# Performance work log

Measured on AMD Instinct MI355X. Metric: run time of the kernel, lower is better.

Reference implementation:

```python
import jax, jax.numpy as jnp
import numpy as np

D = 256
H = 4
HD = D // H


def setup_inputs() -> dict:
    key = jax.random.key(0)
    ks = jax.random.split(key, 12)
    A, T = 64, 512
    s = 1.0 / np.sqrt(D)
    return {
        "features": jax.random.normal(ks[0], (A, T, D), jnp.float32),
        "positions": jax.random.normal(ks[1], (A, T, 2), jnp.float32),
        "Wq": jax.random.normal(ks[2], (D, D), jnp.float32) * s,
        "bq": jnp.zeros((D,), jnp.float32),
        "Wk": jax.random.normal(ks[3], (D, D), jnp.float32) * s,
        "bk": jnp.zeros((D,), jnp.float32),
        "Wv": jax.random.normal(ks[4], (D, D), jnp.float32) * s,
        "bv": jnp.zeros((D,), jnp.float32),
        "Wo": jax.random.normal(ks[5], (D, D), jnp.float32) * s,
        "bo": jnp.zeros((D,), jnp.float32),
        "max_distance": 2,
        "time_window": 64,
    }


def _sparse_mask(positions, max_distance, time_window):
    # positions: [A, T, 2] -> allowed [A, T, T]
    A, T, _ = positions.shape
    diff = positions[:, :, None, :] - positions[:, None, :, :]  # [A,T,T,2]
    dist2 = jnp.sum(diff * diff, axis=-1)                       # [A,T,T]
    t = jnp.arange(T)
    tmask = jnp.abs(t[:, None] - t[None, :]) <= time_window      # [T,T]
    return (dist2 <= float(max_distance) ** 2) & tmask[None]     # [A,T,T]


def reference(features, positions, Wq, bq, Wk, bk, Wv, bv, Wo, bo,
              max_distance, time_window):
    A, T, Dm = features.shape
    allowed = _sparse_mask(positions, max_distance, time_window)  # [A,T,T]
    q = features @ Wq.T + bq
    k = features @ Wk.T + bk
    v = features @ Wv.T + bv
    # split heads: [A, T, H, HD]
    q = q.reshape(A, T, H, HD)
    k = k.reshape(A, T, H, HD)
    v = v.reshape(A, T, H, HD)
    scale = 1.0 / np.sqrt(HD)
    scores = jnp.einsum("athd,ashd->ahts", q, k) * scale          # [A,H,T,T]
    scores = jnp.where(allowed[:, None], scores, -jnp.inf)
    attn = jax.nn.softmax(scores, axis=-1)
    out = jnp.einsum("ahts,ashd->athd", attn, v).reshape(A, T, Dm)
    return out @ Wo.T + bo
```

## Files before the change

kernel.cpp:

```cpp
#include <hip/hip_runtime.h>
#include <hip/hip_bf16.h>
#include <cstdint>
#include <cstddef>

typedef __attribute__((ext_vector_type(8))) _Float16 half8;
typedef __attribute__((ext_vector_type(4))) float floatx4;

#define MFMA16(a, b, c) __builtin_amdgcn_mfma_f32_16x16x32_f16((a), (b), (c), 0, 0, 0)

#define GLOAD_LDS16(g, l)                                                     \
    __builtin_amdgcn_global_load_lds(                                         \
        (const __attribute__((address_space(1))) void*)(g),                   \
        (__attribute__((address_space(3))) void*)(l), 16, 0, 0)

#define NFEAT 8388608

__device__ __forceinline__ void stage_dma(
    const _Float16* __restrict__ src, _Float16* __restrict__ lds,
    int wid, int lane)
{
#pragma unroll
    for (int i = 0; i < 4; ++i) {
        int grp = wid * 4 + i;
        int row = grp * 8 + (lane >> 3);
        int sc  = (lane & 7) ^ (row & 7);
        GLOAD_LDS16(src + (size_t)row * 256 + sc * 8, lds + grp * 512);
    }
}

__device__ __forceinline__ void stage_f32_s(
    const float* __restrict__ src, _Float16* __restrict__ lds, int tid,
    int dst_stride)
{
#pragma unroll
    for (int i = 0; i < 4; ++i) {
        int g   = tid + 256 * i;
        int row = g >> 3, chd = g & 7;
        int chs = chd ^ (row & 7);
        const float* s = src + (size_t)row * 256 + chs * 8;
        float4 v0 = *(const float4*)s;
        float4 v1 = *(const float4*)(s + 4);
        half8 h = { (_Float16)v0.x, (_Float16)v0.y, (_Float16)v0.z, (_Float16)v0.w,
                    (_Float16)v1.x, (_Float16)v1.y, (_Float16)v1.z, (_Float16)v1.w };
        *(half8*)(&lds[row * dst_stride + chd * 8]) = h;
    }
}

__global__ __launch_bounds__(256) void qkv_fused(
    const float* __restrict__ feat,
    const float* __restrict__ Wq, const float* __restrict__ Wk,
    const float* __restrict__ Wv,
    const float* __restrict__ bq, const float* __restrict__ bk,
    const float* __restrict__ bv,
    _Float16* __restrict__ Qb, _Float16* __restrict__ Kb, _Float16* __restrict__ Vb)
{
    __shared__ _Float16 Xs[128 * 256];
    __shared__ _Float16 Ws[128 * 64];

    const int n   = blockIdx.x;
    const int idx = n >> 3;
    const int bm  = (n & 7) * 32 + (idx >> 1);
    const int bn  = idx & 1;

    const int tid  = threadIdx.x;
    const int lane = tid & 63, wid = tid >> 6;
    const int quad = lane >> 4, l16 = lane & 15;
    const int wm = wid & 1, wn = wid >> 1;

    const float* Xg = feat + (size_t)bm * 128 * 256;
#pragma unroll
    for (int slab = 0; slab < 4; ++slab)
        stage_f32_s(Xg + slab * 64, Xs + slab * 64, tid, 256);
    __syncthreads();

#pragma unroll 1
    for (int z = 0; z < 3; ++z) {
        const float* W    = (z == 0) ? Wq : (z == 1) ? Wk : Wv;
        const float* bias = (z == 0) ? bq : (z == 1) ? bk : bv;
        _Float16*    outp = (z == 0) ? Qb : (z == 1) ? Kb : Vb;
        const float* Wg = W + (size_t)bn * 128 * 256;

        floatx4 acc[4][4] = {};
#pragma unroll 1
        for (int ks = 0; ks < 4; ++ks) {
            stage_f32_s(Wg + ks * 64, Ws, tid, 64);
            __syncthreads();
#pragma unroll
            for (int kh = 0; kh < 2; ++kh) {
                half8 af[4], bf[4];
#pragma unroll
                for (int mi = 0; mi < 4; ++mi) {
                    int row = wm * 64 + mi * 16 + l16;
                    int cs  = (kh * 4 + quad) ^ (row & 7);
                    af[mi] = *(const half8*)(&Xs[row * 256 + ks * 64 + cs * 8]);
                }
#pragma unroll
                for (int ni = 0; ni < 4; ++ni) {
                    int row = wn * 64 + ni * 16 + l16;
                    int cs  = (kh * 4 + quad) ^ (row & 7);
                    bf[ni] = *(const half8*)(&Ws[row * 64 + cs * 8]);
                }
#pragma unroll
                for (int mi = 0; mi < 4; ++mi)
#pragma unroll
                    for (int ni = 0; ni < 4; ++ni)
                        acc[mi][ni] = MFMA16(af[mi], bf[ni], acc[mi][ni]);
            }
            __syncthreads();
        }

#pragma unroll
        for (int ni = 0; ni < 4; ++ni) {
            int col = bn * 128 + wn * 64 + ni * 16 + l16;
            float bv2 = bias[col];
#pragma unroll
            for (int mi = 0; mi < 4; ++mi)
#pragma unroll
                for (int r = 0; r < 4; ++r) {
                    int row = bm * 128 + wm * 64 + mi * 16 + quad * 4 + r;
                    outp[(size_t)row * 256 + col] = (_Float16)(acc[mi][ni][r] + bv2);
                }
        }
    }
}

__global__ __launch_bounds__(256) void out_gemm(
    const _Float16* __restrict__ attnH, const float* __restrict__ Wo,
    const float* __restrict__ bo, float* __restrict__ out)
{
    __shared__ _Float16 As[128 * 64];
    __shared__ _Float16 Bs[128 * 64];

    const int n   = blockIdx.x;
    const int idx = n >> 3;
    const int bm  = (n & 7) * 32 + (idx >> 1);
    const int bn  = idx & 1;

    const int tid  = threadIdx.x;
    const int lane = tid & 63, wid = tid >> 6;
    const int quad = lane >> 4, l16 = lane & 15;
    const int wm = wid & 1, wn = wid >> 1;

    floatx4 acc[4][4] = {};
    const float* Wg = Wo + (size_t)bn * 128 * 256;

    for (int k0 = 0; k0 < 256; k0 += 64) {
        stage_dma(attnH + (size_t)bm * 128 * 256 + k0, As, wid, lane);
        stage_f32_s(Wg + k0, Bs, tid, 64);
        __syncthreads();
#pragma unroll
        for (int kh = 0; kh < 2; ++kh) {
            half8 af[4], bf[4];
#pragma unroll
            for (int mi = 0; mi < 4; ++mi) {
                int row = wm * 64 + mi * 16 + l16;
                int cs  = (kh * 4 + quad) ^ (row & 7);
                af[mi] = *(const half8*)(&As[row * 64 + cs * 8]);
            }
#pragma unroll
            for (int ni = 0; ni < 4; ++ni) {
                int row = wn * 64 + ni * 16 + l16;
                int cs  = (kh * 4 + quad) ^ (row & 7);
                bf[ni] = *(const half8*)(&Bs[row * 64 + cs * 8]);
            }
#pragma unroll
            for (int mi = 0; mi < 4; ++mi)
#pragma unroll
                for (int ni = 0; ni < 4; ++ni)
                    acc[mi][ni] = MFMA16(af[mi], bf[ni], acc[mi][ni]);
        }
        __syncthreads();
    }

#pragma unroll
    for (int ni = 0; ni < 4; ++ni) {
        int col = bn * 128 + wn * 64 + ni * 16 + l16;
        float bv = bo[col];
#pragma unroll
        for (int mi = 0; mi < 4; ++mi)
#pragma unroll
            for (int r = 0; r < 4; ++r) {
                int row = bm * 128 + wm * 64 + mi * 16 + quad * 4 + r;
                out[(size_t)row * 256 + col] = acc[mi][ni][r] + bv;
            }
    }
}

__global__ __launch_bounds__(256) void attn_kernel(
    const _Float16* __restrict__ Qb, const _Float16* __restrict__ Kb,
    const _Float16* __restrict__ Vb, const float* __restrict__ positions,
    const int* __restrict__ mdp, const int* __restrict__ twp,
    _Float16* __restrict__ attnb)
{
    const int n   = blockIdx.x;
    const int idx = n >> 3;
    const int a   = (n & 7) * 8 + (idx >> 5);
    const int rem = idx & 31;
    const int qt  = rem >> 2, h = rem & 3;

    const int q0 = qt * 64;
    const int s_base = q0 - 64;
    const int tid = threadIdx.x, lane = tid & 63, wid = tid >> 6;
    const int quad = lane >> 4, l16 = lane & 15;

    __shared__ _Float16 KPs[192 * 64];
    __shared__ _Float16 Vt[64 * 192];

    const size_t abase = (size_t)a * 512;
    const int md = *mdp, tw = *twp;
    const float md2 = (float)(md * md);

    const size_t qrow = abase + q0 + wid * 16 + l16;
    half8 aq0 = *(const half8*)(Qb + qrow * 256 + h * 64 + quad * 8);
    half8 aq1 = *(const half8*)(Qb + qrow * 256 + h * 64 + 32 + quad * 8);
    float qpx[4], qpy[4];
    int trow[4];
#pragma unroll
    for (int r = 0; r < 4; ++r) {
        int m = wid * 16 + quad * 4 + r;
        trow[r] = q0 + m;
        float2 qp = *(const float2*)(positions + (abase + q0 + m) * 2);
        qpx[r] = qp.x;
        qpy[r] = qp.y;
    }

#pragma unroll
    for (int i = 0; i < 6; ++i) {
        int grp = wid * 6 + i;
        int si  = grp * 8 + (lane >> 3);
        int sc  = min(max(s_base + si, 0), 511);
        int ch  = (lane & 7) ^ (si & 7);
        GLOAD_LDS16(Kb + (abase + sc) * 256 + h * 64 + ch * 8, KPs + grp * 512);
    }
#pragma unroll
    for (int i = 0; i < 3; ++i) {
        int g   = tid + 256 * i;
        int si2 = (g % 96) * 2;
        int d0  = (g / 96) * 8;
        int sa  = min(max(s_base + si2, 0), 511);
        int sb  = min(max(s_base + si2 + 1, 0), 511);
        half8 v0 = *(const half8*)(Vb + (abase + sa) * 256 + h * 64 + d0);
        half8 v1 = *(const half8*)(Vb + (abase + sb) * 256 + h * 64 + d0);
        int c = si2 >> 3;
#pragma unroll
        for (int j = 0; j < 8; ++j) {
            int d  = d0 + j;
            int cs = (c & ~7) | ((c & 7) ^ (d & 7));
            union { _Float16 hh[2]; uint32_t u; } p;
            p.hh[0] = v0[j]; p.hh[1] = v1[j];
            *(uint32_t*)(&Vt[d * 192 + cs * 8 + (si2 & 7)]) = p.u;
        }
    }
    __syncthreads();

    floatx4 S[12];
#pragma unroll
    for (int j = 0; j < 12; ++j) {
        int si = j * 16 + l16;
        half8 bk0 = *(const half8*)(&KPs[si * 64 + ((quad) ^ (si & 7)) * 8]);
        half8 bk1 = *(const half8*)(&KPs[si * 64 + ((4 + quad) ^ (si & 7)) * 8]);
        floatx4 acc = {};
        acc = MFMA16(aq0, bk0, acc);
        acc = MFMA16(aq1, bk1, acc);
        int sr = s_base + si;
        int sc = min(max(sr, 0), 511);
        float2 kp = *(const float2*)(positions + (abase + sc) * 2);
        bool svalid = (sr >= 0) && (sr < 512);
#pragma unroll
        for (int r = 0; r < 4; ++r) {
            float dx = qpx[r] - kp.x, dy = qpy[r] - kp.y;
            float d2 = dx * dx + dy * dy;
            int dt = trow[r] - sr; dt = dt < 0 ? -dt : dt;
            bool ok = svalid && (d2 <= md2) && (dt <= tw);
            S[j][r] = ok ? acc[r] * 0.125f : -1e30f;
        }
    }

    float minv[4];
#pragma unroll
    for (int r = 0; r < 4; ++r) {
        float m = -1e30f;
#pragma unroll
        for (int j = 0; j < 12; ++j) m = fmaxf(m, S[j][r]);
        m = fmaxf(m, __shfl_xor(m, 1));
        m = fmaxf(m, __shfl_xor(m, 2));
        m = fmaxf(m, __shfl_xor(m, 4));
        m = fmaxf(m, __shfl_xor(m, 8));
        float l = 0.f;
#pragma unroll
        for (int j = 0; j < 12; ++j) {
            float p = __expf(S[j][r] - m);
            S[j][r] = p;
            l += p;
        }
        l += __shfl_xor(l, 1);
        l += __shfl_xor(l, 2);
        l += __shfl_xor(l, 4);
        l += __shfl_xor(l, 8);
        minv[r] = 1.0f / l;
    }

    __syncthreads();

    _Float16* Ps = KPs + wid * (16 * 192);
#pragma unroll
    for (int j = 0; j < 12; ++j)
#pragma unroll
        for (int r = 0; r < 4; ++r) {
            int row = quad * 4 + r;
            int col = j * 16 + l16;
            int ch  = (col >> 3) ^ (row & 7);
            Ps[row * 192 + ch * 8 + (col & 7)] = (_Float16)(S[j][r] * minv[r]);
        }

    half8 af[6];
#pragma unroll
    for (int k = 0; k < 6; ++k) {
        int ch = (k * 4 + quad) ^ (l16 & 7);
        af[k] = *(const half8*)(&Ps[l16 * 192 + ch * 8]);
    }
#pragma unroll
    for (int nn = 0; nn < 4; ++nn) {
        floatx4 accO = {};
#pragma unroll
        for (int k = 0; k < 6; ++k) {
            int row = nn * 16 + l16;
            int c   = k * 4 + quad;
            int cs  = (c & ~7) | ((c & 7) ^ (row & 7));
            half8 bv = *(const half8*)(&Vt[row * 192 + cs * 8]);
            accO = MFMA16(af[k], bv, accO);
        }
#pragma unroll
        for (int r = 0; r < 4; ++r) {
            int row = q0 + wid * 16 + quad * 4 + r;
            attnb[(abase + row) * 256 + h * 64 + nn * 16 + l16] = (_Float16)accO[r];
        }
    }
}

extern "C" void kernel_launch(void* const* d_in, const int* in_sizes, int n_in,
                              void* d_out, int out_size, void* d_ws, size_t ws_size,
                              hipStream_t stream)
{
    const float* feat = (const float*)d_in[0];
    const float* pos  = (const float*)d_in[1];
    const float* Wq   = (const float*)d_in[2];
    const float* bq   = (const float*)d_in[3];
    const float* Wk   = (const float*)d_in[4];
    const float* bk   = (const float*)d_in[5];
    const float* Wv   = (const float*)d_in[6];
    const float* bv   = (const float*)d_in[7];
    const float* Wo   = (const float*)d_in[8];
    const float* bo   = (const float*)d_in[9];
    const int*   md   = (const int*)d_in[10];
    const int*   tw   = (const int*)d_in[11];
    float*       out  = (float*)d_out;

    _Float16* ws    = (_Float16*)d_ws;
    _Float16* Qb    = ws;
    _Float16* Kb    = Qb + NFEAT;
    _Float16* Vb    = Kb + NFEAT;
    _Float16* attnH = Vb + NFEAT;

    qkv_fused<<<512, 256, 0, stream>>>(feat, Wq, Wk, Wv, bq, bk, bv, Qb, Kb, Vb);

    attn_kernel<<<2048, 256, 0, stream>>>(Qb, Kb, Vb, pos, md, tw, attnH);

    out_gemm<<<512, 256, 0, stream>>>(attnH, Wo, bo, out);
}
```

Baseline: 167.7 us.

## Software-pipeline weight tile loads through registers in QKV and output GEMMs

```diff
diff --git a/kernel.cpp b/kernel.cpp
--- a/kernel.cpp
+++ b/kernel.cpp
@@ -14,37 +14,6 @@
         (__attribute__((address_space(3))) void*)(l), 16, 0, 0)
 
 #define NFEAT 8388608
-
-__device__ __forceinline__ void stage_dma(
-    const _Float16* __restrict__ src, _Float16* __restrict__ lds,
-    int wid, int lane)
-{
-#pragma unroll
-    for (int i = 0; i < 4; ++i) {
-        int grp = wid * 4 + i;
-        int row = grp * 8 + (lane >> 3);
-        int sc  = (lane & 7) ^ (row & 7);
-        GLOAD_LDS16(src + (size_t)row * 256 + sc * 8, lds + grp * 512);
-    }
-}
-
-__device__ __forceinline__ void stage_f32_s(
-    const float* __restrict__ src, _Float16* __restrict__ lds, int tid,
-    int dst_stride)
-{
-#pragma unroll
-    for (int i = 0; i < 4; ++i) {
-        int g   = tid + 256 * i;
-        int row = g >> 3, chd = g & 7;
-        int chs = chd ^ (row & 7);
-        const float* s = src + (size_t)row * 256 + chs * 8;
-        float4 v0 = *(const float4*)s;
-        float4 v1 = *(const float4*)(s + 4);
-        half8 h = { (_Float16)v0.x, (_Float16)v0.y, (_Float16)v0.z, (_Float16)v0.w,
-                    (_Float16)v1.x, (_Float16)v1.y, (_Float16)v1.z, (_Float16)v1.w };
-        *(half8*)(&lds[row * dst_stride + chd * 8]) = h;
-    }
-}
 
 __global__ __launch_bounds__(256) void qkv_fused(
     const float* __restrict__ feat,
@@ -54,7 +23,7 @@
     const float* __restrict__ bv,
     _Float16* __restrict__ Qb, _Float16* __restrict__ Kb, _Float16* __restrict__ Vb)
 {
-    __shared__ _Float16 Xs[128 * 256];
+    __shared__ _Float16 Xs[4 * 128 * 64];
     __shared__ _Float16 Ws[128 * 64];
 
     const int n   = blockIdx.x;
@@ -69,57 +38,105 @@
 
     const float* Xg = feat + (size_t)bm * 128 * 256;
 #pragma unroll
-    for (int slab = 0; slab < 4; ++slab)
-        stage_f32_s(Xg + slab * 64, Xs + slab * 64, tid, 256);
-    __syncthreads();
+    for (int sl = 0; sl < 4; ++sl)
+#pragma unroll
+        for (int i = 0; i < 4; ++i) {
+            int g   = tid + 256 * i;
+            int row = g >> 3, chd = g & 7;
+            int chs = chd ^ (row & 7);
+            const float* s = Xg + (size_t)row * 256 + sl * 64 + chs * 8;
+            float4 v0 = *(const float4*)s;
+            float4 v1 = *(const float4*)(s + 4);
+            half8 h = { (_Float16)v0.x, (_Float16)v0.y, (_Float16)v0.z, (_Float16)v0.w,
+                        (_Float16)v1.x, (_Float16)v1.y, (_Float16)v1.z, (_Float16)v1.w };
+            *(half8*)(&Xs[sl * 8192 + row * 64 + chd * 8]) = h;
+        }
+
+    const float* Wz[3] = { Wq, Wk, Wv };
+    const float* bz[3] = { bq, bk, bv };
+    _Float16*    oz[3] = { Qb, Kb, Vb };
+
+    int wrow[4], wchd[4];
+#pragma unroll
+    for (int i = 0; i < 4; ++i) {
+        int g = tid + 256 * i;
+        wrow[i] = g >> 3;
+        wchd[i] = g & 7;
+    }
+    float4 pv0[4], pv1[4];
+
+    auto loadW = [&](int t) {
+        const float* base = Wz[t >> 2] + (size_t)bn * 32768 + (t & 3) * 64;
+#pragma unroll
+        for (int i = 0; i < 4; ++i) {
+            int chs = wchd[i] ^ (wrow[i] & 7);
+            const float* s = base + (size_t)wrow[i] * 256 + chs * 8;
+            pv0[i] = *(const float4*)s;
+            pv1[i] = *(const float4*)(s + 4);
+        }
+    };
+    auto storeW = [&]() {
+#pragma unroll
+        for (int i = 0; i < 4; ++i) {
+            half8 h = { (_Float16)pv0[i].x, (_Float16)pv0[i].y,
+                        (_Float16)pv0[i].z, (_Float16)pv0[i].w,
+                        (_Float16)pv1[i].x, (_Float16)pv1[i].y,
+                        (_Float16)pv1[i].z, (_Float16)pv1[i].w };
+            *(half8*)(&Ws[wrow[i] * 64 + wchd[i] * 8]) = h;
+        }
+    };
+
+    loadW(0);
+    storeW();
+    floatx4 acc[4][4] = {};
 
 #pragma unroll 1
-    for (int z = 0; z < 3; ++z) {
-        const float* W    = (z == 0) ? Wq : (z == 1) ? Wk : Wv;
-        const float* bias = (z == 0) ? bq : (z == 1) ? bk : bv;
-        _Float16*    outp = (z == 0) ? Qb : (z == 1) ? Kb : Vb;
-        const float* Wg = W + (size_t)bn * 128 * 256;
-
-        floatx4 acc[4][4] = {};
-#pragma unroll 1
-        for (int ks = 0; ks < 4; ++ks) {
-            stage_f32_s(Wg + ks * 64, Ws, tid, 64);
-            __syncthreads();
-#pragma unroll
-            for (int kh = 0; kh < 2; ++kh) {
-                half8 af[4], bf[4];
+    for (int t = 0; t < 12; ++t) {
+        __syncthreads();
+        if (t < 11) loadW(t + 1);
+        const int ks = t & 3;
+#pragma unroll
+        for (int kh = 0; kh < 2; ++kh) {
+            half8 af[4], bf[4];
+#pragma unroll
+            for (int mi = 0; mi < 4; ++mi) {
+                int row = wm * 64 + mi * 16 + l16;
+                int cs  = (kh * 4 + quad) ^ (row & 7);
+                af[mi] = *(const half8*)(&Xs[ks * 8192 + row * 64 + cs * 8]);
+            }
+#pragma unroll
+            for (int ni = 0; ni < 4; ++ni) {
+                int row = wn * 64 + ni * 16 + l16;
+                int cs  = (kh * 4 + quad) ^ (row & 7);
+                bf[ni] = *(const half8*)(&Ws[row * 64 + cs * 8]);
+            }
+#pragma unroll
+            for (int mi = 0; mi < 4; ++mi)
+#pragma unroll
+                for (int ni = 0; ni < 4; ++ni)
+                    acc[mi][ni] = MFMA16(af[mi], bf[ni], acc[mi][ni]);
+        }
+        __syncthreads();
+        if (t < 11) storeW();
+        if ((t & 3) == 3) {
+            const int z = t >> 2;
+            const float* bias = bz[z];
+            _Float16*    outp = oz[z];
+#pragma unroll
+            for (int ni = 0; ni < 4; ++ni) {
+                int col = bn * 128 + wn * 64 + ni * 16 + l16;
+                float bv2 = bias[col];
 #pragma unroll
                 for (int mi = 0; mi < 4; ++mi) {
-                    int row = wm * 64 + mi * 16 + l16;
-                    int cs  = (kh * 4 + quad) ^ (row & 7);
-                    af[mi] = *(const half8*)(&Xs[row * 256 + ks * 64 + cs * 8]);
+#pragma unroll
+                    for (int r = 0; r < 4; ++r) {
+                        int row = bm * 128 + wm * 64 + mi * 16 + quad * 4 + r;
+                        outp[(size_t)row * 256 + col] =
+                            (_Float16)(acc[mi][ni][r] + bv2);
+                    }
+                    acc[mi][ni] = floatx4{0.f, 0.f, 0.f, 0.f};
                 }
-#pragma unroll
-                for (int ni = 0; ni < 4; ++ni) {
-                    int row = wn * 64 + ni * 16 + l16;
-                    int cs  = (kh * 4 + quad) ^ (row & 7);
-                    bf[ni] = *(const half8*)(&Ws[row * 64 + cs * 8]);
-                }
-#pragma unroll
-                for (int mi = 0; mi < 4; ++mi)
-#pragma unroll
-                    for (int ni = 0; ni < 4; ++ni)
-                        acc[mi][ni] = MFMA16(af[mi], bf[ni], acc[mi][ni]);
-            }
-            __syncthreads();
-        }
-
-#pragma unroll
-        for (int ni = 0; ni < 4; ++ni) {
-            int col = bn * 128 + wn * 64 + ni * 16 + l16;
-            float bv2 = bias[col];
-#pragma unroll
-            for (int mi = 0; mi < 4; ++mi)
-#pragma unroll
-                for (int r = 0; r < 4; ++r) {
-                    int row = bm * 128 + wm * 64 + mi * 16 + quad * 4 + r;
-                    outp[(size_t)row * 256 + col] = (_Float16)(acc[mi][ni][r] + bv2);
-                }
+            }
         }
     }
 }
@@ -128,8 +145,8 @@
     const _Float16* __restrict__ attnH, const float* __restrict__ Wo,
     const float* __restrict__ bo, float* __restrict__ out)
 {
-    __shared__ _Float16 As[128 * 64];
-    __shared__ _Float16 Bs[128 * 64];
+    __shared__ _Float16 Xs[4 * 128 * 64];
+    __shared__ _Float16 Ws[128 * 64];
 
     const int n   = blockIdx.x;
     const int idx = n >> 3;
@@ -141,13 +158,56 @@
     const int quad = lane >> 4, l16 = lane & 15;
     const int wm = wid & 1, wn = wid >> 1;
 
+    const _Float16* Ag = attnH + (size_t)bm * 128 * 256;
+#pragma unroll
+    for (int sl = 0; sl < 4; ++sl)
+#pragma unroll
+        for (int i = 0; i < 4; ++i) {
+            int grp = wid * 4 + i;
+            int row = grp * 8 + (lane >> 3);
+            int sc  = (lane & 7) ^ (row & 7);
+            GLOAD_LDS16(Ag + (size_t)row * 256 + sl * 64 + sc * 8,
+                        Xs + sl * 8192 + grp * 512);
+        }
+
+    int wrow[4], wchd[4];
+#pragma unroll
+    for (int i = 0; i < 4; ++i) {
+        int g = tid + 256 * i;
+        wrow[i] = g >> 3;
+        wchd[i] = g & 7;
+    }
+    float4 pv0[4], pv1[4];
+
+    auto loadW = [&](int t) {
+        const float* base = Wo + (size_t)bn * 32768 + t * 64;
+#pragma unroll
+        for (int i = 0; i < 4; ++i) {
+            int chs = wchd[i] ^ (wrow[i] & 7);
+            const float* s = base + (size_t)wrow[i] * 256 + chs * 8;
+            pv0[i] = *(const float4*)s;
+            pv1[i] = *(const float4*)(s + 4);
+        }
+    };
+    auto storeW = [&]() {
+#pragma unroll
+        for (int i = 0; i < 4; ++i) {
+            half8 h = { (_Float16)pv0[i].x, (_Float16)pv0[i].y,
+                        (_Float16)pv0[i].z, (_Float16)pv0[i].w,
+                        (_Float16)pv1[i].x, (_Float16)pv1[i].y,
+                        (_Float16)pv1[i].z, (_Float16)pv1[i].w };
+            *(half8*)(&Ws[wrow[i] * 64 + wchd[i] * 8]) = h;
+        }
+    };
+
+    loadW(0);
+    storeW();
     floatx4 acc[4][4] = {};
-    const float* Wg = Wo + (size_t)bn * 128 * 256;
-
-    for (int k0 = 0; k0 < 256; k0 += 64) {
-        stage_dma(attnH + (size_t)bm * 128 * 256 + k0, As, wid, lane);
-        stage_f32_s(Wg + k0, Bs, tid, 64);
+
+#pragma unroll 1
+    for (int t = 0; t < 4; ++t) {
         __syncthreads();
+        if (t < 3) loadW(t + 1);
 #pragma unroll
         for (int kh = 0; kh < 2; ++kh) {
             half8 af[4], bf[4];
@@ -155,13 +215,13 @@
             for (int mi = 0; mi < 4; ++mi) {
                 int row = wm * 64 + mi * 16 + l16;
                 int cs  = (kh * 4 + quad) ^ (row & 7);
-                af[mi] = *(const half8*)(&As[row * 64 + cs * 8]);
+                af[mi] = *(const half8*)(&Xs[t * 8192 + row * 64 + cs * 8]);
             }
 #pragma unroll
             for (int ni = 0; ni < 4; ++ni) {
                 int row = wn * 64 + ni * 16 + l16;
                 int cs  = (kh * 4 + quad) ^ (row & 7);
-                bf[ni] = *(const half8*)(&Bs[row * 64 + cs * 8]);
+                bf[ni] = *(const half8*)(&Ws[row * 64 + cs * 8]);
             }
 #pragma unroll
             for (int mi = 0; mi < 4; ++mi)
@@ -170,6 +230,7 @@
                     acc[mi][ni] = MFMA16(af[mi], bf[ni], acc[mi][ni]);
         }
         __syncthreads();
+        if (t < 3) storeW();
     }
 
 #pragma unroll
```

Measured after the change: 170.1 us. No clear change (+1.5%).
